# Optimization experiments

Measured on AMD Instinct MI355X. Metric: run time of the kernel, lower is better.

Reference implementation:

```python
import jax, jax.numpy as jnp
import numpy as np

N_DIRS = 32  # number of projection directions


def gram_schmidt(x):
    # x: [B, n, D]; sequential Gram-Schmidt; normalized basis vectors are
    # detached (stop_gradient) as in the torch original.
    B, n, D = x.shape
    xs = jnp.swapaxes(x, 0, 1)  # [n, B, D]
    basis0 = jnp.zeros((n, B, D), dtype=x.dtype)

    def step(carry, w):
        basis, i = carry

        def proj(j, wv):
            b = basis[j]  # rows >= i are zero and contribute nothing
            return wv - b * jnp.sum(wv * b, axis=-1, keepdims=True)

        w_o = jax.lax.fori_loop(0, n, proj, w)
        w_sg = jax.lax.stop_gradient(w_o)
        w_hat = w_sg / jnp.linalg.norm(w_sg, axis=-1, keepdims=True)
        basis = jax.lax.dynamic_update_slice(basis, w_hat[None], (i, 0, 0))
        return (basis, i + 1), w_o

    (_, _), x_orth = jax.lax.scan(step, (basis0, jnp.int32(0)), xs)
    return jnp.swapaxes(x_orth, 0, 1)  # [B, n, D]


def setup_inputs() -> dict:
    key = jax.random.key(0)
    k = jax.random.split(key, 6)
    B = 2048
    IN_LP = 32 * 26       # 832 = linear_projection_x_dim * 26
    IMG = 28 * 28         # 784
    IN_NET = 2 * IMG      # 1568
    OUT_NET = N_DIRS * IMG  # 25088

    x_distorted = jax.random.normal(k[0], (B, IN_LP), dtype=jnp.float32)
    x_restored = jax.random.uniform(k[1], (B, 1, 28, 28), dtype=jnp.float32)

    s1 = 1.0 / np.sqrt(IN_LP)
    W_lp = jax.random.uniform(k[2], (IMG, IN_LP), jnp.float32, -s1, s1)
    b_lp = jax.random.uniform(k[3], (IMG,), jnp.float32, -s1, s1)

    s2 = 1.0 / np.sqrt(IN_NET)
    W_net = jax.random.uniform(k[4], (OUT_NET, IN_NET), jnp.float32, -s2, s2)
    b_net = jax.random.uniform(k[5], (OUT_NET,), jnp.float32, -s2, s2)

    return {"x_distorted": x_distorted, "x_restored": x_restored,
            "W_lp": W_lp, "b_lp": b_lp, "W_net": W_net, "b_net": b_net}


def reference(x_distorted, x_restored, W_lp, b_lp, W_net, b_net):
    B = x_distorted.shape[0]
    xd = x_distorted.reshape(B, -1) @ W_lp.T + b_lp      # [B, 784]
    xd = xd.reshape(B, 1, 28, 28)
    x = jnp.concatenate([xd, x_restored], axis=1)        # [B, 2, 28, 28]
    x = (x - 0.5) / 0.2
    w_mat = (x.reshape(B, -1) @ W_net.T + b_net) * 0.2   # [B, n_dirs*784]
    w_mat = w_mat.reshape(B, N_DIRS, -1)                 # [B, n_dirs, 784]
    return gram_schmidt(w_mat)
```

## Files before the change

kernel.cpp:

```cpp
#include <hip/hip_runtime.h>
#include <hip/hip_bf16.h>
#include <stdint.h>


typedef short s16x8 __attribute__((ext_vector_type(8)));
typedef float f32x4 __attribute__((ext_vector_type(4)));

#define GL_LDS16(gptr, lptr)                                                   \
    __builtin_amdgcn_global_load_lds(                                          \
        (const __attribute__((address_space(1))) void*)(gptr),                 \
        (__attribute__((address_space(3))) void*)(lptr), 16, 0, 0)

#define KP 1600

__global__ __launch_bounds__(512, 1) void gemm_mfma_256(
    const __hip_bfloat16* __restrict__ A, const __hip_bfloat16* __restrict__ B,
    const float* __restrict__ bias, float* __restrict__ C,
    int M, int N, int K)
{
    __shared__ __align__(16) short lds[2][30720];

    const int t = threadIdx.x;
    const int l = t & 63;
    const int wv = t >> 6;
    const int wm = wv >> 1;
    const int wn = wv & 1;

    const int f  = blockIdx.x;
    const int xb = f >> 3;
    const int yb = f & 7;
    const int m0 = yb * 256;
    const int n0 = xb * 224;

    const short* As = (const short*)A;
    const short* Bs = (const short*)B;

    const bool isA = wv < 4;
    const int colE = (((l & 7) ^ (l >> 3)) << 3);
    const size_t srcRow = isA ? (size_t)(m0 + wv * 64 + (l >> 3))
                              : (size_t)(n0 + (wv - 4) * 56 + (l >> 3));
    const size_t src0 = srcRow * KP + colE;
    const short* gsrc = isA ? As : Bs;
    const int dstBase = isA ? wv * 4096 : 16384 + (wv - 4) * 3584;

    const int sk0 = ((l >> 4) << 3) ^ ((l & 7) << 3);
    const int sk1 = sk0 ^ 32;
    const int aoff = (wm * 64 + (l & 15)) * 64;
    const int boff = 16384 + (wn * 112 + (l & 15)) * 64;

    f32x4 acc[4][7] = {};

#define STAGE_TILE(buf, T)                                                     \
    do {                                                                       \
        short* d_ = &lds[buf][dstBase];                                        \
        const short* s_ = gsrc + src0 + (size_t)(T) * 64;                      \
        GL_LDS16(s_ + (size_t)0 * 8 * KP, d_ + 0 * 512);                       \
        GL_LDS16(s_ + (size_t)1 * 8 * KP, d_ + 1 * 512);                       \
        GL_LDS16(s_ + (size_t)2 * 8 * KP, d_ + 2 * 512);                       \
        GL_LDS16(s_ + (size_t)3 * 8 * KP, d_ + 3 * 512);                       \
        GL_LDS16(s_ + (size_t)4 * 8 * KP, d_ + 4 * 512);                       \
        GL_LDS16(s_ + (size_t)5 * 8 * KP, d_ + 5 * 512);                       \
        GL_LDS16(s_ + (size_t)6 * 8 * KP, d_ + 6 * 512);                       \
        if (isA) GL_LDS16(s_ + (size_t)7 * 8 * KP, d_ + 7 * 512);              \
    } while (0)

    const int NT = K >> 6;
    STAGE_TILE(0, 0);
    __syncthreads();

    for (int kt = 0; kt < NT; ++kt) {
        const int cur = kt & 1;
        const short* bufc = &lds[cur][0];

        if (kt + 1 < NT) STAGE_TILE(cur ^ 1, kt + 1);

        s16x8 bfr[7][2];
        #pragma unroll
        for (int ni = 0; ni < 7; ++ni) {
            bfr[ni][0] = *(const s16x8*)&bufc[boff + ni * 1024 + sk0];
            bfr[ni][1] = *(const s16x8*)&bufc[boff + ni * 1024 + sk1];
        }

        #pragma unroll
        for (int mi = 0; mi < 4; ++mi) {
            s16x8 a0 = *(const s16x8*)&bufc[aoff + mi * 1024 + sk0];
            s16x8 a1 = *(const s16x8*)&bufc[aoff + mi * 1024 + sk1];
            __builtin_amdgcn_s_setprio(1);
            #pragma unroll
            for (int ni = 0; ni < 7; ++ni) {
                acc[mi][ni] = __builtin_amdgcn_mfma_f32_16x16x32_bf16(
                    a0, bfr[ni][0], acc[mi][ni], 0, 0, 0);
                acc[mi][ni] = __builtin_amdgcn_mfma_f32_16x16x32_bf16(
                    a1, bfr[ni][1], acc[mi][ni], 0, 0, 0);
            }
            __builtin_amdgcn_s_setprio(0);
        }

        __syncthreads();
    }
#undef STAGE_TILE

    const int row0 = m0 + wm * 64 + ((l >> 4) << 2);
    const int col0 = n0 + wn * 112 + (l & 15);
    #pragma unroll
    for (int ni = 0; ni < 7; ++ni) {
        const int n = col0 + ni * 16;
        const float bn = bias[n];
        #pragma unroll
        for (int mi = 0; mi < 4; ++mi) {
            const int r0 = row0 + mi * 16;
            #pragma unroll
            for (int r = 0; r < 4; ++r)
                C[(size_t)(r0 + r) * N + n] = (acc[mi][ni][r] + bn) * 0.2f;
        }
    }
}

#define TILE_M 64
#define TILE_N 64
#define TILE_K 16
#define LDS_STRIDE 72
#define NB_K1 416
#define NB_K2 2048
#define NB_K0 25088

__global__ __launch_bounds__(256) void prep012(
    const float* __restrict__ xd, const float* __restrict__ xr,
    const float* __restrict__ Wlp, const float* __restrict__ blp,
    const float* __restrict__ Wnet,
    __hip_bfloat16* __restrict__ Wnet_bf, __hip_bfloat16* __restrict__ x_bf)
{
    const int bid = blockIdx.x;
    const int t = threadIdx.x;

    if (bid < NB_K1) {
        __shared__ float As[TILE_K][LDS_STRIDE];
        __shared__ float Bsh[TILE_K][LDS_STRIDE];

        const int bx = bid % 13, by = bid / 13;
        const int tx = t & 15;
        const int ty = t >> 4;
        const int m0 = by * TILE_M;
        const int n0 = bx * TILE_N;
        const int lrow = t >> 2;
        const int lk   = (t & 3) << 2;
        const int Kd = 832, Nd = 784;

        float acc[4][4] = {};

        for (int kt = 0; kt < Kd; kt += TILE_K) {
            float4 av = *(const float4*)(xd + (size_t)(m0 + lrow) * Kd + kt + lk);
            float4 bv = make_float4(0.f, 0.f, 0.f, 0.f);
            if (n0 + lrow < Nd)
                bv = *(const float4*)(Wlp + (size_t)(n0 + lrow) * Kd + kt + lk);

            __syncthreads();
            As[lk + 0][lrow] = av.x; As[lk + 1][lrow] = av.y;
            As[lk + 2][lrow] = av.z; As[lk + 3][lrow] = av.w;
            Bsh[lk + 0][lrow] = bv.x; Bsh[lk + 1][lrow] = bv.y;
            Bsh[lk + 2][lrow] = bv.z; Bsh[lk + 3][lrow] = bv.w;
            __syncthreads();

            #pragma unroll
            for (int k = 0; k < TILE_K; ++k) {
                float4 a = *(const float4*)&As[k][ty << 2];
                float4 b = *(const float4*)&Bsh[k][tx << 2];
                acc[0][0] += a.x * b.x; acc[0][1] += a.x * b.y;
                acc[0][2] += a.x * b.z; acc[0][3] += a.x * b.w;
                acc[1][0] += a.y * b.x; acc[1][1] += a.y * b.y;
                acc[1][2] += a.y * b.z; acc[1][3] += a.y * b.w;
                acc[2][0] += a.z * b.x; acc[2][1] += a.z * b.y;
                acc[2][2] += a.z * b.z; acc[2][3] += a.z * b.w;
                acc[3][0] += a.w * b.x; acc[3][1] += a.w * b.y;
                acc[3][2] += a.w * b.z; acc[3][3] += a.w * b.w;
            }
        }

        #pragma unroll
        for (int j = 0; j < 4; ++j) {
            int n = n0 + (tx << 2) + j;
            if (n < Nd) {
                float bn = blp[n];
                #pragma unroll
                for (int i = 0; i < 4; ++i) {
                    float v = (acc[i][j] + bn - 0.5f) / 0.2f;
                    x_bf[(size_t)(m0 + (ty << 2) + i) * KP + n] =
                        __float2bfloat16(v);
                }
            }
        }
    } else if (bid < NB_K1 + NB_K2) {
        const int b = bid - NB_K1;
        if (t < 196) {
            float4 v = *(const float4*)(xr + (size_t)b * 784 + (t << 2));
            __hip_bfloat16 o[4] = {
                __float2bfloat16((v.x - 0.5f) / 0.2f),
                __float2bfloat16((v.y - 0.5f) / 0.2f),
                __float2bfloat16((v.z - 0.5f) / 0.2f),
                __float2bfloat16((v.w - 0.5f) / 0.2f)};
            *(ushort4*)&x_bf[(size_t)b * KP + 784 + (t << 2)] =
                *(const ushort4*)o;
        } else if (t < 204) {
            *(ushort4*)&x_bf[(size_t)b * KP + 1568 + ((t - 196) << 2)] =
                make_ushort4(0, 0, 0, 0);
        }
    } else {
        const size_t r = bid - (NB_K1 + NB_K2);
        const float* src = Wnet + r * 1568;
        __hip_bfloat16* dst = Wnet_bf + r * KP;

        for (int i = t; i < 392; i += 256) {
            float4 v = *(const float4*)(src + (i << 2));
            __hip_bfloat16 o[4] = {
                __float2bfloat16(v.x), __float2bfloat16(v.y),
                __float2bfloat16(v.z), __float2bfloat16(v.w)};
            *(ushort4*)&dst[i << 2] = *(const ushort4*)o;
        }
        if (t < 8)
            *(ushort4*)&dst[1568 + (t << 2)] = make_ushort4(0, 0, 0, 0);
    }
}

#define GS_N 32
#define GS_D 784

__device__ __forceinline__ s16x8 cvt8(float4 a, float4 b) {
    __hip_bfloat16 h[8] = {
        __float2bfloat16(a.x), __float2bfloat16(a.y),
        __float2bfloat16(a.z), __float2bfloat16(a.w),
        __float2bfloat16(b.x), __float2bfloat16(b.y),
        __float2bfloat16(b.z), __float2bfloat16(b.w)};
    return *(const s16x8*)h;
}

__global__ __launch_bounds__(256, 4) void gram_solve(
    const float* __restrict__ out, float* __restrict__ Mws)
{
    __shared__ float Gs[GS_N][GS_N + 1];
    __shared__ float Ms[GS_N][GS_N + 1];
    __shared__ float Ld[GS_N];

    const int t = threadIdx.x;
    const int l = t & 63;
    const int w = t >> 6;
    const float* row0 = out + (size_t)blockIdx.x * (GS_N * GS_D);

    const int wr = w >> 1, wc2 = w & 1;
    const int ra = wr * 16 + (l & 15);
    const int rb = wc2 * 16 + (l & 15);
    const int kg = l >> 4;

    const float* pa = row0 + (size_t)ra * GS_D + kg * 8;
    const float* pb = row0 + (size_t)rb * GS_D + kg * 8;

    f32x4 acc = {};
    #pragma unroll 2
    for (int s = 0; s < 24; ++s) {
        float4 a0 = *(const float4*)(pa + s * 32);
        float4 a1 = *(const float4*)(pa + s * 32 + 4);
        float4 b0 = *(const float4*)(pb + s * 32);
        float4 b1 = *(const float4*)(pb + s * 32 + 4);
        acc = __builtin_amdgcn_mfma_f32_16x16x32_bf16(
            cvt8(a0, a1), cvt8(b0, b1), acc, 0, 0, 0);
    }
    {
        s16x8 af = {}, bf = {};
        if (kg < 2) {
            float4 a0 = *(const float4*)(pa + 768);
            float4 a1 = *(const float4*)(pa + 768 + 4);
            float4 b0 = *(const float4*)(pb + 768);
            float4 b1 = *(const float4*)(pb + 768 + 4);
            af = cvt8(a0, a1); bf = cvt8(b0, b1);
        }
        acc = __builtin_amdgcn_mfma_f32_16x16x32_bf16(af, bf, acc, 0, 0, 0);
    }

    {
        const int di = wr * 16 + (l >> 4) * 4;
        const int dj = wc2 * 16 + (l & 15);
        #pragma unroll
        for (int r = 0; r < 4; ++r) Gs[di + r][dj] = acc[r];
    }
    for (int z = t; z < GS_N * (GS_N + 1); z += 256) ((float*)Ms)[z] = 0.f;
    __syncthreads();

    for (int k = 0; k < GS_N; ++k) {
        const float sk = sqrtf(Gs[k][k]);
        if (t == k) Ld[k] = sk;
        if (t > k && t < GS_N) Gs[t][k] /= sk;
        __syncthreads();
        if (t > k && t < GS_N) {
            const float lik = Gs[t][k];
            for (int j = k + 1; j <= t; ++j)
                Gs[t][j] -= lik * Gs[j][k];
        }
        __syncthreads();
    }

    if (t < GS_N) {
        const int j = t;
        Ms[j][j] = 1.0f / Ld[j];
        for (int i = j + 1; i < GS_N; ++i) {
            float a = 0.f;
            for (int k = j; k < i; ++k)
                a += Gs[i][k] * Ms[k][j];
            Ms[i][j] = -a / Ld[i];
        }
        for (int i = j + 1; i < GS_N; ++i)
            Ms[i][j] *= Ld[i];
    }
    __syncthreads();

    {
        const int i = t >> 3, j0 = (t & 7) << 2;
        float4 mv = make_float4(Ms[i][j0], Ms[i][j0 + 1],
                                Ms[i][j0 + 2], Ms[i][j0 + 3]);
        *(float4*)(Mws + (size_t)blockIdx.x * 1024 + (t << 2)) = mv;
    }
}

__global__ __launch_bounds__(256, 8) void gs_apply(
    float* __restrict__ out, const float* __restrict__ Mws)
{
    __shared__ float4 Wf[GS_N][28];
    __shared__ float  Ml[GS_N][36];

    const int t = threadIdx.x;
    const int b = blockIdx.y;
    const int k0 = blockIdx.x * 112;
    float* row0 = out + (size_t)b * (GS_N * GS_D);

    {
        float4 mv = *(const float4*)(Mws + (size_t)b * 1024 + (t << 2));
        const int i = t >> 3, j0 = (t & 7) << 2;
        *(float4*)&Ml[i][j0] = mv;
    }
    #pragma unroll
    for (int hh = 0; hh < 4; ++hh) {
        const int h = t + hh * 256;
        const int r = h >> 5, c = h & 31;
        if (c < 28)
            Wf[r][c] = *(const float4*)(row0 + r * GS_D + k0 + (c << 2));
    }
    __syncthreads();

    const int g  = t >> 5;
    const int c4 = t & 31;
    if (c4 < 28) {
        const int rA = g, rB = 31 - g, rC = 15 - g, rD = 16 + g;
        float4 vA = Wf[rA][c4];
        float4 vB = Wf[rB][c4];
        float4 vC = Wf[rC][c4];
        float4 vD = Wf[rD][c4];
        for (int j = 0; j < rB; ++j) {
            const float4 wj = Wf[j][c4];
            const float mA = (j < rA) ? Ml[rA][j] : 0.f;
            const float mB = Ml[rB][j];
            vA.x += mA * wj.x; vA.y += mA * wj.y;
            vA.z += mA * wj.z; vA.w += mA * wj.w;
            vB.x += mB * wj.x; vB.y += mB * wj.y;
            vB.z += mB * wj.z; vB.w += mB * wj.w;
        }
        for (int j = 0; j < rD; ++j) {
            const float4 wj = Wf[j][c4];
            const float mC = (j < rC) ? Ml[rC][j] : 0.f;
            const float mD = Ml[rD][j];
            vC.x += mC * wj.x; vC.y += mC * wj.y;
            vC.z += mC * wj.z; vC.w += mC * wj.w;
            vD.x += mD * wj.x; vD.y += mD * wj.y;
            vD.z += mD * wj.z; vD.w += mD * wj.w;
        }
        *(float4*)(row0 + rA * GS_D + k0 + (c4 << 2)) = vA;
        *(float4*)(row0 + rB * GS_D + k0 + (c4 << 2)) = vB;
        *(float4*)(row0 + rC * GS_D + k0 + (c4 << 2)) = vC;
        *(float4*)(row0 + rD * GS_D + k0 + (c4 << 2)) = vD;
    }
}

extern "C" void kernel_launch(void* const* d_in, const int* in_sizes, int n_in,
                              void* d_out, int out_size, void* d_ws, size_t ws_size,
                              hipStream_t stream)
{
    const float* xd   = (const float*)d_in[0];
    const float* xr   = (const float*)d_in[1];
    const float* Wlp  = (const float*)d_in[2];
    const float* blp  = (const float*)d_in[3];
    const float* Wnet = (const float*)d_in[4];
    const float* bnet = (const float*)d_in[5];
    float* out = (float*)d_out;

    const int B = 2048, OUT = 32 * 784;

    __hip_bfloat16* Wnet_bf = (__hip_bfloat16*)d_ws;
    __hip_bfloat16* x_bf =
        (__hip_bfloat16*)((char*)d_ws + (size_t)OUT * KP * 2);
    float* Mws = (float*)d_ws;

    prep012<<<NB_K1 + NB_K2 + NB_K0, 256, 0, stream>>>(
        xd, xr, Wlp, blp, Wnet, Wnet_bf, x_bf);

    gemm_mfma_256<<<dim3(896), 512, 0, stream>>>(
        x_bf, Wnet_bf, bnet, out, B, OUT, KP);

    gram_solve<<<B, 256, 0, stream>>>(out, Mws);

    gs_apply<<<dim3(7, B), 256, 0, stream>>>(out, Mws);
}
```

Baseline: 440.9 us.

## Stage Gram-matrix inputs through double-buffered swizzled LDS in gram_solve

The Gram product in gram_solve used to read each row straight from global memory, so several waves fetched the same rows again. Each block now copies 64-column chunks of its 32x784 slab into LDS with global_load_lds. The copies are double-buffered across 12 chunks and use an XOR swizzle to avoid bank conflicts, and the MFMA operands are read from LDS. Launch bounds go from 4 to 6 blocks per SM. The change adds 16KB of LDS and a barrier per chunk, and the extra blocks per SM could press on registers or LDS.

```diff
diff --git a/kernel.cpp b/kernel.cpp
--- a/kernel.cpp
+++ b/kernel.cpp
@@ -233,9 +233,10 @@
     return *(const s16x8*)h;
 }
 
-__global__ __launch_bounds__(256, 4) void gram_solve(
+__global__ __launch_bounds__(256, 6) void gram_solve(
     const float* __restrict__ out, float* __restrict__ Mws)
 {
+    __shared__ __align__(16) float Wb[2][GS_N * 64];
     __shared__ float Gs[GS_N][GS_N + 1];
     __shared__ float Ms[GS_N][GS_N + 1];
     __shared__ float Ld[GS_N];
@@ -250,22 +251,51 @@
     const int rb = wc2 * 16 + (l & 15);
     const int kg = l >> 4;
 
-    const float* pa = row0 + (size_t)ra * GS_D + kg * 8;
-    const float* pb = row0 + (size_t)rb * GS_D + kg * 8;
+    const int rb0 = w * 8, rb1 = w * 8 + 4;
+    const int lr  = l >> 4;
+    const int lc0 = (l & 15) ^ ((rb0 & 15) + lr);
+    const int lc1 = (l & 15) ^ ((rb1 & 15) + lr);
+    const size_t s0 = (size_t)(rb0 + lr) * GS_D + lc0 * 4;
+    const size_t s1 = (size_t)(rb1 + lr) * GS_D + lc1 * 4;
+    const int d0 = rb0 * 64;
+    const int d1 = rb1 * 64;
+
+#define GSTAGE(buf, c)                                                         \
+    do {                                                                       \
+        GL_LDS16(row0 + s0 + (c) * 64, &Wb[buf][d0]);                          \
+        GL_LDS16(row0 + s1 + (c) * 64, &Wb[buf][d1]);                          \
+    } while (0)
 
     f32x4 acc = {};
-    #pragma unroll 2
-    for (int s = 0; s < 24; ++s) {
-        float4 a0 = *(const float4*)(pa + s * 32);
-        float4 a1 = *(const float4*)(pa + s * 32 + 4);
-        float4 b0 = *(const float4*)(pb + s * 32);
-        float4 b1 = *(const float4*)(pb + s * 32 + 4);
-        acc = __builtin_amdgcn_mfma_f32_16x16x32_bf16(
-            cvt8(a0, a1), cvt8(b0, b1), acc, 0, 0, 0);
-    }
+    GSTAGE(0, 0);
+    __syncthreads();
+
+    const int pa0 = ra * 64;
+    const int pb0 = rb * 64;
+    const int ma = ra & 15, mb = rb & 15;
+
+    for (int c = 0; c < 12; ++c) {
+        const float* buf = Wb[c & 1];
+        if (c < 11) GSTAGE((c + 1) & 1, c + 1);
+        #pragma unroll
+        for (int s = 0; s < 2; ++s) {
+            const int ca = 8 * s + 2 * kg;
+            float4 a0 = *(const float4*)&buf[pa0 + ((ca    ) ^ ma) * 4];
+            float4 a1 = *(const float4*)&buf[pa0 + ((ca + 1) ^ ma) * 4];
+            float4 b0 = *(const float4*)&buf[pb0 + ((ca    ) ^ mb) * 4];
+            float4 b1 = *(const float4*)&buf[pb0 + ((ca + 1) ^ mb) * 4];
+            acc = __builtin_amdgcn_mfma_f32_16x16x32_bf16(
+                cvt8(a0, a1), cvt8(b0, b1), acc, 0, 0, 0);
+        }
+        __syncthreads();
+    }
+#undef GSTAGE
+
     {
         s16x8 af = {}, bf = {};
         if (kg < 2) {
+            const float* pa = row0 + (size_t)ra * GS_D + kg * 8;
+            const float* pb = row0 + (size_t)rb * GS_D + kg * 8;
             float4 a0 = *(const float4*)(pa + 768);
             float4 a1 = *(const float4*)(pa + 768 + 4);
             float4 b0 = *(const float4*)(pb + 768);
```

Result: slower. 456.6 us (+3.6%).
